# Performance work log

Measured on AMD Instinct MI355X. Metric: run time of the kernel, lower is better.

## Reference

```python
import jax, jax.numpy as jnp
import numpy as np

B, S, Lb, C, CP, H = 64, 4, 64, 32, 16, 4
LN_EPS = 1e-5


def layer_norm(x, g, b):
    mu = jnp.mean(x, axis=-1, keepdims=True)
    var = jnp.mean(jnp.square(x - mu), axis=-1, keepdims=True)
    return (x - mu) * jax.lax.rsqrt(var + LN_EPS) * g + b


def mha(x, w_in, b_in, w_out, b_out, h):
    # torch nn.MultiheadAttention, batch_first, self-attention
    Bx, L, Cx = x.shape
    d = Cx // h
    qkv = x @ w_in.T + b_in                      # (Bx, L, 3C)
    q, k, v = jnp.split(qkv, 3, axis=-1)
    sp = lambda t: t.reshape(Bx, L, h, d).transpose(0, 2, 1, 3)  # (Bx,h,L,d)
    q, k, v = sp(q), sp(k), sp(v)
    scale = 1.0 / jnp.sqrt(jnp.asarray(d, x.dtype))
    attn = jax.nn.softmax(jnp.einsum('bhid,bhjd->bhij', q, k) * scale, axis=-1)
    o = jnp.einsum('bhij,bhjd->bhid', attn, v).transpose(0, 2, 1, 3).reshape(Bx, L, Cx)
    return o @ w_out.T + b_out


def setup_inputs() -> dict:
    key = jax.random.key(0)
    ks = jax.random.split(key, 20)
    g = lambda i, shape, s=0.05: (jax.random.normal(ks[i], shape, dtype=jnp.float32) * s)
    inp = {
        'chip_ctcf': jax.random.normal(ks[0], (B, Lb), dtype=jnp.float32),
        'chip_hac':  jax.random.normal(ks[1], (B, Lb), dtype=jnp.float32),
        'chip_me1':  jax.random.normal(ks[2], (B, Lb), dtype=jnp.float32),
        'chip_me3':  jax.random.normal(ks[3], (B, Lb), dtype=jnp.float32),
        'embed_w': g(4, (C, 1)), 'embed_b': g(5, (C,)),
        'pos_embed': g(6, (1, 1, Lb, C), 0.02),
        'row_in_w': g(7, (3 * C, C)), 'row_in_b': g(8, (3 * C,)),
        'row_out_w': g(9, (C, C)), 'row_out_b': g(10, (C,)),
        'row_ln_g': jnp.ones((C,), jnp.float32), 'row_ln_b': jnp.zeros((C,), jnp.float32),
        'col_in_w': g(11, (3 * C, C)), 'col_in_b': g(12, (3 * C,)),
        'col_out_w': g(13, (C, C)), 'col_out_b': g(14, (C,)),
        'col_ln_g': jnp.ones((C,), jnp.float32), 'col_ln_b': jnp.zeros((C,), jnp.float32),
        'proj_w': g(15, (CP, C * C)), 'proj_b': g(16, (CP,)),
        'pln_g': jnp.ones((CP,), jnp.float32), 'pln_b': jnp.zeros((CP,), jnp.float32),
    }
    return inp


def reference(chip_ctcf, chip_hac, chip_me1, chip_me3,
              embed_w, embed_b, pos_embed,
              row_in_w, row_in_b, row_out_w, row_out_b, row_ln_g, row_ln_b,
              col_in_w, col_in_b, col_out_w, col_out_b, col_ln_g, col_ln_b,
              proj_w, proj_b, pln_g, pln_b):
    Bv = chip_ctcf.shape[0]
    signals = jnp.stack([chip_ctcf, chip_hac, chip_me1, chip_me3], axis=1)  # (B,4,64)
    # Linear(1, C): scalar embed
    msa = signals[..., None] * embed_w[:, 0] + embed_b                      # (B,4,64,C)
    msa = msa + pos_embed
    # row attention over the 64 bins, per track
    x = msa.reshape(Bv * S, Lb, C)
    x = layer_norm(x + mha(x, row_in_w, row_in_b, row_out_w, row_out_b, H), row_ln_g, row_ln_b)
    msa = x.reshape(Bv, S, Lb, C)
    # column attention over the 4 tracks, per bin
    x = msa.transpose(0, 2, 1, 3).reshape(Bv * Lb, S, C)
    x = layer_norm(x + mha(x, col_in_w, col_in_b, col_out_w, col_out_b, H), col_ln_g, col_ln_b)
    msa = x.reshape(Bv, Lb, S, C).transpose(0, 2, 1, 3)                     # (B,4,64,C)
    # outer product of the track-mean (as written in the torch source)
    m = jnp.mean(msa, axis=1)                                               # (B,64,C)
    pair = jnp.einsum('bic,bjd->bijcd', m, m).reshape(Bv, Lb, Lb, C * C)    # (B,64,64,1024)
    nrm = jnp.sqrt(jnp.sum(jnp.square(pair), axis=-1, keepdims=True))
    pair = pair / jnp.maximum(nrm, 1e-6)                                    # F.normalize eps=1e-6
    feat = pair @ proj_w.T + proj_b                                         # (B,64,64,CP)
    feat = layer_norm(feat, pln_g, pln_b)
    feat = feat * jax.nn.sigmoid(feat)                                      # SiLU
    return feat.transpose(0, 3, 1, 2)                                       # (B,CP,64,64)
```

## Files before the change

kernel.cpp:

```cpp
#include <hip/hip_runtime.h>
#include <hip/hip_cooperative_groups.h>

namespace cg = cooperative_groups;

#define LN_EPS 1e-5f

__device__ __forceinline__ float dot8(float4 a0, float4 a1, float4 b0, float4 b1) {
    return a0.x * b0.x + a0.y * b0.y + a0.z * b0.z + a0.w * b0.w +
           a1.x * b1.x + a1.y * b1.y + a1.z * b1.z + a1.w * b1.w;
}

__global__ __launch_bounds__(512, 4) void k_fused(
    const float* __restrict__ ctcf, const float* __restrict__ hac,
    const float* __restrict__ me1,  const float* __restrict__ me3,
    const float* __restrict__ ew,   const float* __restrict__ eb,
    const float* __restrict__ pe,
    const float* __restrict__ riw,  const float* __restrict__ rib,
    const float* __restrict__ row_w,const float* __restrict__ row_b,
    const float* __restrict__ rlg,  const float* __restrict__ rlb,
    const float* __restrict__ ciw,  const float* __restrict__ cib,
    const float* __restrict__ cow,  const float* __restrict__ cob,
    const float* __restrict__ clg,  const float* __restrict__ clb,
    const float* __restrict__ pw,   const float* __restrict__ pb,
    const float* __restrict__ pg,   const float* __restrict__ pbt,
    float* msaR, float* mbuf, float* nbuf, float* out)
{
    __shared__ float smem[7552];
    const int bx  = blockIdx.x;
    const int tid = threadIdx.x;
    cg::grid_group grid = cg::this_grid();

    {
        float* sqkv = smem;
        float* so   = smem + 6400;

        const int qh = bx & 1, s = (bx >> 1) & 3, b = bx >> 3;
        const int qbase = qh * 32;
        const float* chip = (s == 0) ? ctcf : (s == 1) ? hac : (s == 2) ? me1 : me3;
        const int l   = tid & 63;
        const int cgi = __builtin_amdgcn_readfirstlane(tid >> 6);

        float xr[32];
        {
            const float cv = chip[b * 64 + l];
            const float4* pe4 = (const float4*)&pe[l * 32];
            const float4* ew4 = (const float4*)ew;
            const float4* eb4 = (const float4*)eb;
#pragma unroll
            for (int c4 = 0; c4 < 8; ++c4) {
                float4 pv = pe4[c4], e = ew4[c4], bb = eb4[c4];
                xr[c4 * 4 + 0] = cv * e.x + bb.x + pv.x;
                xr[c4 * 4 + 1] = cv * e.y + bb.y + pv.y;
                xr[c4 * 4 + 2] = cv * e.z + bb.z + pv.z;
                xr[c4 * 4 + 3] = cv * e.w + bb.w + pv.w;
            }
        }

        {
            const int cc0 = cgi * 12;
            float acc[12];
#pragma unroll
            for (int ii = 0; ii < 12; ++ii) acc[ii] = rib[cc0 + ii];
#pragma unroll
            for (int ii = 0; ii < 12; ++ii) {
                const float4* wr4 = (const float4*)&riw[(cc0 + ii) * 32];
#pragma unroll
                for (int c4 = 0; c4 < 8; ++c4) {
                    float4 wv = wr4[c4];
                    acc[ii] += xr[c4 * 4 + 0] * wv.x + xr[c4 * 4 + 1] * wv.y +
                               xr[c4 * 4 + 2] * wv.z + xr[c4 * 4 + 3] * wv.w;
                }
            }
            float* dst = &sqkv[l * 100 + cc0];
            *(float4*)(dst + 0) = make_float4(acc[0], acc[1], acc[2],  acc[3]);
            *(float4*)(dst + 4) = make_float4(acc[4], acc[5], acc[6],  acc[7]);
            *(float4*)(dst + 8) = make_float4(acc[8], acc[9], acc[10], acc[11]);
        }
        __syncthreads();

        {
            const int h  = tid >> 7;
            const int q  = (tid >> 2) & 31;
            const int kc = tid & 3;
            const int lq = qbase + q;
            const float4* qp = (const float4*)&sqkv[lq * 100 + h * 8];
            float4 q0 = qp[0], q1 = qp[1];
            const float scale = 0.35355339059327373f;

            float sc[16];
#pragma unroll
            for (int jj = 0; jj < 16; ++jj) {
                const int j = kc * 16 + ((jj + kc) & 15);
                const float4* kp = (const float4*)&sqkv[j * 100 + 32 + h * 8];
                sc[jj] = dot8(q0, q1, kp[0], kp[1]) * scale;
            }
            float m0 = fmaxf(fmaxf(fmaxf(sc[0], sc[1]),  fmaxf(sc[2], sc[3])),
                             fmaxf(fmaxf(sc[4], sc[5]),  fmaxf(sc[6], sc[7])));
            float m1 = fmaxf(fmaxf(fmaxf(sc[8], sc[9]),  fmaxf(sc[10], sc[11])),
                             fmaxf(fmaxf(sc[12], sc[13]), fmaxf(sc[14], sc[15])));
            float mx = fmaxf(m0, m1);
            mx = fmaxf(mx, __shfl_xor(mx, 1, 64));
            mx = fmaxf(mx, __shfl_xor(mx, 2, 64));

            float den = 0.f, a[8];
#pragma unroll
            for (int dd = 0; dd < 8; ++dd) a[dd] = 0.f;
#pragma unroll
            for (int jj = 0; jj < 16; ++jj) {
                const int j = kc * 16 + ((jj + kc) & 15);
                float wgt = __expf(sc[jj] - mx);
                den += wgt;
                const float4* vp = (const float4*)&sqkv[j * 100 + 64 + h * 8];
                float4 v0 = vp[0], v1 = vp[1];
                a[0] += wgt * v0.x;  a[1] += wgt * v0.y;
                a[2] += wgt * v0.z;  a[3] += wgt * v0.w;
                a[4] += wgt * v1.x;  a[5] += wgt * v1.y;
                a[6] += wgt * v1.z;  a[7] += wgt * v1.w;
            }
#pragma unroll
            for (int off = 1; off <= 2; off <<= 1) {
                den += __shfl_xor(den, off, 64);
#pragma unroll
                for (int dd = 0; dd < 8; ++dd) a[dd] += __shfl_xor(a[dd], off, 64);
            }
            float inv = 1.f / den;
            float r0, r1;
            if      (kc == 0) { r0 = a[0]; r1 = a[1]; }
            else if (kc == 1) { r0 = a[2]; r1 = a[3]; }
            else if (kc == 2) { r0 = a[4]; r1 = a[5]; }
            else              { r0 = a[6]; r1 = a[7]; }
            so[q * 36 + h * 8 + kc * 2 + 0] = r0 * inv;
            so[q * 36 + h * 8 + kc * 2 + 1] = r1 * inv;
        }
        __syncthreads();

        {
            const int lq2 = tid & 31;
            const int cB  = tid >> 5;
            const int lg  = qbase + lq2;
            const float cvr = chip[b * 64 + lg];
            float orow[32];
            const float4* sop = (const float4*)&so[lq2 * 36];
#pragma unroll
            for (int k4 = 0; k4 < 8; ++k4) {
                float4 t = sop[k4];
                orow[k4 * 4 + 0] = t.x;  orow[k4 * 4 + 1] = t.y;
                orow[k4 * 4 + 2] = t.z;  orow[k4 * 4 + 3] = t.w;
            }
#pragma unroll
            for (int i = 0; i < 2; ++i) {
                int c = cB + i * 16;
                const float4* wr4 = (const float4*)&row_w[c * 32];
                float acc = row_b[c] + (cvr * ew[c] + eb[c] + pe[lg * 32 + c]);
#pragma unroll
                for (int k4 = 0; k4 < 8; ++k4) {
                    float4 wv = wr4[k4];
                    acc += orow[k4 * 4 + 0] * wv.x + orow[k4 * 4 + 1] * wv.y +
                           orow[k4 * 4 + 2] * wv.z + orow[k4 * 4 + 3] * wv.w;
                }
                sqkv[lq2 * 100 + c] = acc;
            }
        }
        __syncthreads();

        {
            const int c = tid & 31;
#pragma unroll
            for (int p = 0; p < 2; ++p) {
                int r = p * 16 + (tid >> 5);
                float v = sqkv[r * 100 + c];
                float s1 = v;
#pragma unroll
                for (int off = 16; off >= 1; off >>= 1) s1 += __shfl_xor(s1, off, 64);
                float mu = s1 * (1.f / 32.f);
                float d = v - mu;
                float s2 = d * d;
#pragma unroll
                for (int off = 16; off >= 1; off >>= 1) s2 += __shfl_xor(s2, off, 64);
                float rstd = rsqrtf(s2 * (1.f / 32.f) + LN_EPS);
                msaR[((b * 4 + s) * 64 + qbase + r) * 32 + c] =
                    d * rstd * rlg[c] + rlb[c];
            }
        }
    }
    grid.sync();

    {
        float* sx2   = smem;
        float* sqkv2 = smem + 1056;
        float* so2   = smem + 4256;

        const int b  = bx >> 3;
        const int l0 = (bx & 7) * 8;

        for (int n = tid; n < 1024; n += 512) {
            int r = n >> 5, c = n & 31;
            int lo = r >> 2, s = r & 3;
            sx2[r * 33 + c] = msaR[((b * 4 + s) * 64 + l0 + lo) * 32 + c];
        }
        __syncthreads();

        {
            const int rr = tid & 31;
            const int cg2 = tid >> 5;
            float xr[32];
#pragma unroll
            for (int c = 0; c < 32; ++c) xr[c] = sx2[rr * 33 + c];
#pragma unroll
            for (int i = 0; i < 6; ++i) {
                int cc = i * 16 + cg2;
                const float4* wr4 = (const float4*)&ciw[cc * 32];
                float acc = cib[cc];
#pragma unroll
                for (int c4 = 0; c4 < 8; ++c4) {
                    float4 wv = wr4[c4];
                    acc += xr[c4 * 4 + 0] * wv.x + xr[c4 * 4 + 1] * wv.y +
                           xr[c4 * 4 + 2] * wv.z + xr[c4 * 4 + 3] * wv.w;
                }
                sqkv2[rr * 100 + cc] = acc;
            }
        }
        __syncthreads();

        if (tid < 128) {
            const int lo = tid >> 4, h = (tid >> 2) & 3, ia = tid & 3;
            const float scale = 0.35355339059327373f;
            const float4* qp = (const float4*)&sqkv2[(lo * 4 + ia) * 100 + h * 8];
            float4 q0 = qp[0], q1 = qp[1];
            float sc[4];
            float mx = -1e30f;
#pragma unroll
            for (int jj = 0; jj < 4; ++jj) {
                const float4* kp = (const float4*)&sqkv2[(lo * 4 + jj) * 100 + 32 + h * 8];
                sc[jj] = dot8(q0, q1, kp[0], kp[1]) * scale;
                mx = fmaxf(mx, sc[jj]);
            }
            float den = 0.f;
#pragma unroll
            for (int jj = 0; jj < 4; ++jj) { sc[jj] = __expf(sc[jj] - mx); den += sc[jj]; }
            float inv = 1.f / den;
            float a[8];
#pragma unroll
            for (int dd = 0; dd < 8; ++dd) a[dd] = 0.f;
#pragma unroll
            for (int jj = 0; jj < 4; ++jj) {
                const float4* vp = (const float4*)&sqkv2[(lo * 4 + jj) * 100 + 64 + h * 8];
                float4 v0 = vp[0], v1 = vp[1];
                float wgt = sc[jj];
                a[0] += wgt * v0.x;  a[1] += wgt * v0.y;
                a[2] += wgt * v0.z;  a[3] += wgt * v0.w;
                a[4] += wgt * v1.x;  a[5] += wgt * v1.y;
                a[6] += wgt * v1.z;  a[7] += wgt * v1.w;
            }
#pragma unroll
            for (int dd = 0; dd < 8; ++dd) so2[(lo * 4 + ia) * 36 + h * 8 + dd] = a[dd] * inv;
        }
        __syncthreads();

        {
            const int r2 = tid & 31;
            const int cB = tid >> 5;
            float orow[32];
            const float4* sop = (const float4*)&so2[r2 * 36];
#pragma unroll
            for (int k4 = 0; k4 < 8; ++k4) {
                float4 t = sop[k4];
                orow[k4 * 4 + 0] = t.x;  orow[k4 * 4 + 1] = t.y;
                orow[k4 * 4 + 2] = t.z;  orow[k4 * 4 + 3] = t.w;
            }
#pragma unroll
            for (int i = 0; i < 2; ++i) {
                int c = cB + i * 16;
                const float4* wr4 = (const float4*)&cow[c * 32];
                float acc = cob[c] + sx2[r2 * 33 + c];
#pragma unroll
                for (int k4 = 0; k4 < 8; ++k4) {
                    float4 wv = wr4[k4];
                    acc += orow[k4 * 4 + 0] * wv.x + orow[k4 * 4 + 1] * wv.y +
                           orow[k4 * 4 + 2] * wv.z + orow[k4 * 4 + 3] * wv.w;
                }
                sqkv2[r2 * 100 + c] = acc;
            }
        }
        __syncthreads();

        {
            const int c = tid & 31;
#pragma unroll
            for (int p = 0; p < 2; ++p) {
                int r = p * 16 + (tid >> 5);
                float v = sqkv2[r * 100 + c];
                float s1 = v;
#pragma unroll
                for (int off = 16; off >= 1; off >>= 1) s1 += __shfl_xor(s1, off, 64);
                float mu = s1 * (1.f / 32.f);
                float d = v - mu;
                float s2 = d * d;
#pragma unroll
                for (int off = 16; off >= 1; off >>= 1) s2 += __shfl_xor(s2, off, 64);
                float rstd = rsqrtf(s2 * (1.f / 32.f) + LN_EPS);
                so2[r * 36 + c] = d * rstd;
            }
        }
        __syncthreads();

        if (tid < 256) {
            const int lo = tid >> 5, c = tid & 31;
            float mval = 0.25f * (so2[(lo * 4 + 0) * 36 + c] + so2[(lo * 4 + 1) * 36 + c] +
                                  so2[(lo * 4 + 2) * 36 + c] + so2[(lo * 4 + 3) * 36 + c]) *
                         clg[c] + clb[c];
            mbuf[(b * 64 + l0 + lo) * 32 + c] = mval;
            float q2 = mval * mval;
#pragma unroll
            for (int off = 16; off >= 1; off >>= 1) q2 += __shfl_xor(q2, off, 64);
            if (c == 0) nbuf[b * 64 + l0 + lo] = sqrtf(q2);
        }
    }
    grid.sync();

    {
        float* smj = smem;
        float* sT  = smem + 2304;
        float* snj = smem + 6464;
        float* sb  = smem + 6528;
        float* sg  = smem + 6544;
        float* sbt = smem + 6560;

        const int b  = bx >> 3;
        const int i0 = (bx & 7) * 8;
        const int lane = tid & 63, w = tid >> 6;

        const float* pwp = pw + (tid >> 5) * 1024 + (tid & 31);
        float w0[32];
#pragma unroll
        for (int c = 0; c < 32; ++c) w0[c] = pwp[c * 32];

        const float* mb = mbuf + b * 2048;
        for (int n = tid; n < 2048; n += 512) smj[(n >> 5) * 36 + (n & 31)] = mb[n];
        if (tid < 64) snj[tid] = nbuf[b * 64 + tid];
        if (tid < 16) { sb[tid] = pb[tid]; sg[tid] = pg[tid]; sbt[tid] = pbt[tid]; }
        __syncthreads();

#pragma unroll
        for (int il = 0; il < 8; ++il) {
            const float4* mr4 = (const float4*)&smj[(i0 + il) * 36];
            float a0 = 0.f;
#pragma unroll
            for (int c4 = 0; c4 < 8; ++c4) {
                float4 mv = mr4[c4];
                a0 += mv.x * w0[c4 * 4 + 0] + mv.y * w0[c4 * 4 + 1] +
                      mv.z * w0[c4 * 4 + 2] + mv.w * w0[c4 * 4 + 3];
            }
            sT[il * 520 + tid] = a0;
        }
        __syncthreads();

        const int j = lane;
        float mj[32];
        {
            const float4* mjp = (const float4*)&smj[j * 36];
#pragma unroll
            for (int d4 = 0; d4 < 8; ++d4) {
                float4 t = mjp[d4];
                mj[d4 * 4 + 0] = t.x;  mj[d4 * 4 + 1] = t.y;
                mj[d4 * 4 + 2] = t.z;  mj[d4 * 4 + 3] = t.w;
            }
        }
        const float nj = snj[j];
        const int il = w;
        const int ig = i0 + il;
        const float invn = 1.f / fmaxf(snj[ig] * nj, 1e-6f);
        float f[16];
#pragma unroll
        for (int cp = 0; cp < 16; ++cp) {
            const float4* tr = (const float4*)&sT[il * 520 + cp * 32];
            float acc = 0.f;
#pragma unroll
            for (int d4 = 0; d4 < 8; ++d4) {
                float4 tv = tr[d4];
                acc += tv.x * mj[d4 * 4 + 0] + tv.y * mj[d4 * 4 + 1] +
                       tv.z * mj[d4 * 4 + 2] + tv.w * mj[d4 * 4 + 3];
            }
            f[cp] = acc * invn + sb[cp];
        }
        float mu = 0.f;
#pragma unroll
        for (int cp = 0; cp < 16; ++cp) mu += f[cp];
        mu *= (1.f / 16.f);
        float var = 0.f;
#pragma unroll
        for (int cp = 0; cp < 16; ++cp) { float d = f[cp] - mu; var += d * d; }
        var *= (1.f / 16.f);
        const float rstd = rsqrtf(var + LN_EPS);
#pragma unroll
        for (int cp = 0; cp < 16; ++cp) {
            float v = (f[cp] - mu) * rstd * sg[cp] + sbt[cp];
            float sl = v / (1.f + __expf(-v));
            out[((b * 16 + cp) * 64 + ig) * 64 + j] = sl;
        }
    }
}

__global__ __launch_bounds__(512, 4) void k_row(
    const float* __restrict__ ctcf, const float* __restrict__ hac,
    const float* __restrict__ me1,  const float* __restrict__ me3,
    const float* __restrict__ ew,   const float* __restrict__ eb,
    const float* __restrict__ pe,
    const float* __restrict__ w_in, const float* __restrict__ b_in,
    const float* __restrict__ w_out,const float* __restrict__ b_out,
    const float* __restrict__ ln_g, const float* __restrict__ ln_b,
    float* __restrict__ msaR)
{
    __shared__ float sx[64][33];
    __shared__ float sqkv[64 * 100];
    __shared__ float so[32][33];

    const int blk = blockIdx.x;
    const int qh  = blk & 1;
    const int s   = (blk >> 1) & 3;
    const int b   = blk >> 3;
    const int qbase = qh * 32;
    const int tid = threadIdx.x;

    const float* chip = (s == 0) ? ctcf : (s == 1) ? hac : (s == 2) ? me1 : me3;

    const int l  = tid & 63;
    const int cg = __builtin_amdgcn_readfirstlane(tid >> 6);

    float xr[32];
    {
        const float cv = chip[b * 64 + l];
        const float4* pe4 = (const float4*)&pe[l * 32];
        const float4* ew4 = (const float4*)ew;
        const float4* eb4 = (const float4*)eb;
#pragma unroll
        for (int c4 = 0; c4 < 8; ++c4) {
            float4 pv = pe4[c4], e = ew4[c4], bb = eb4[c4];
            xr[c4 * 4 + 0] = cv * e.x + bb.x + pv.x;
            xr[c4 * 4 + 1] = cv * e.y + bb.y + pv.y;
            xr[c4 * 4 + 2] = cv * e.z + bb.z + pv.z;
            xr[c4 * 4 + 3] = cv * e.w + bb.w + pv.w;
        }
    }
    if (cg == 0) {
#pragma unroll
        for (int c = 0; c < 32; ++c) sx[l][c] = xr[c];
    }

#pragma unroll
    for (int i = 0; i < 12; ++i) {
        const int cc = i * 8 + cg;
        const float4* wr4 = (const float4*)&w_in[cc * 32];
        float acc = b_in[cc];
#pragma unroll
        for (int c4 = 0; c4 < 8; ++c4) {
            float4 wv = wr4[c4];
            acc += xr[c4 * 4 + 0] * wv.x + xr[c4 * 4 + 1] * wv.y +
                   xr[c4 * 4 + 2] * wv.z + xr[c4 * 4 + 3] * wv.w;
        }
        sqkv[l * 100 + cc] = acc;
    }
    __syncthreads();

    {
        const int h  = tid >> 7;
        const int q  = (tid >> 2) & 31;
        const int kc = tid & 3;
        const int lq = qbase + q;
        const float4* qp = (const float4*)&sqkv[lq * 100 + h * 8];
        float4 q0 = qp[0], q1 = qp[1];
        const float scale = 0.35355339059327373f;

        float sc[16];
#pragma unroll
        for (int jj = 0; jj < 16; ++jj) {
            const int j = kc * 16 + ((jj + kc) & 15);
            const float4* kp = (const float4*)&sqkv[j * 100 + 32 + h * 8];
            sc[jj] = dot8(q0, q1, kp[0], kp[1]) * scale;
        }
        float m0 = fmaxf(fmaxf(fmaxf(sc[0], sc[1]),  fmaxf(sc[2], sc[3])),
                         fmaxf(fmaxf(sc[4], sc[5]),  fmaxf(sc[6], sc[7])));
        float m1 = fmaxf(fmaxf(fmaxf(sc[8], sc[9]),  fmaxf(sc[10], sc[11])),
                         fmaxf(fmaxf(sc[12], sc[13]), fmaxf(sc[14], sc[15])));
        float mx = fmaxf(m0, m1);
        mx = fmaxf(mx, __shfl_xor(mx, 1, 64));
        mx = fmaxf(mx, __shfl_xor(mx, 2, 64));

        float den = 0.f, a[8];
#pragma unroll
        for (int dd = 0; dd < 8; ++dd) a[dd] = 0.f;
#pragma unroll
        for (int jj = 0; jj < 16; ++jj) {
            const int j = kc * 16 + ((jj + kc) & 15);
            float w = __expf(sc[jj] - mx);
            den += w;
            const float4* vp = (const float4*)&sqkv[j * 100 + 64 + h * 8];
            float4 v0 = vp[0], v1 = vp[1];
            a[0] += w * v0.x;  a[1] += w * v0.y;
            a[2] += w * v0.z;  a[3] += w * v0.w;
            a[4] += w * v1.x;  a[5] += w * v1.y;
            a[6] += w * v1.z;  a[7] += w * v1.w;
        }
#pragma unroll
        for (int off = 1; off <= 2; off <<= 1) {
            den += __shfl_xor(den, off, 64);
#pragma unroll
            for (int dd = 0; dd < 8; ++dd) a[dd] += __shfl_xor(a[dd], off, 64);
        }
        float inv = 1.f / den;
        float r0, r1;
        if      (kc == 0) { r0 = a[0]; r1 = a[1]; }
        else if (kc == 1) { r0 = a[2]; r1 = a[3]; }
        else if (kc == 2) { r0 = a[4]; r1 = a[5]; }
        else              { r0 = a[6]; r1 = a[7]; }
        so[q][h * 8 + kc * 2 + 0] = r0 * inv;
        so[q][h * 8 + kc * 2 + 1] = r1 * inv;
    }
    __syncthreads();

    {
        const int lq2 = tid & 31;
        const int cB  = tid >> 5;
        float orow[32];
#pragma unroll
        for (int k = 0; k < 32; ++k) orow[k] = so[lq2][k];
#pragma unroll
        for (int i = 0; i < 2; ++i) {
            int c = cB + i * 16;
            const float4* wr4 = (const float4*)&w_out[c * 32];
            float acc = b_out[c] + sx[qbase + lq2][c];
#pragma unroll
            for (int k4 = 0; k4 < 8; ++k4) {
                float4 wv = wr4[k4];
                acc += orow[k4 * 4 + 0] * wv.x + orow[k4 * 4 + 1] * wv.y +
                       orow[k4 * 4 + 2] * wv.z + orow[k4 * 4 + 3] * wv.w;
            }
            sqkv[lq2 * 100 + c] = acc;
        }
    }
    __syncthreads();

    {
        const int c = tid & 31;
#pragma unroll
        for (int p = 0; p < 2; ++p) {
            int r = p * 16 + (tid >> 5);
            float v = sqkv[r * 100 + c];
            float s1 = v;
#pragma unroll
            for (int off = 16; off >= 1; off >>= 1) s1 += __shfl_xor(s1, off, 64);
            float mu = s1 * (1.f / 32.f);
            float d = v - mu;
            float s2 = d * d;
#pragma unroll
            for (int off = 16; off >= 1; off >>= 1) s2 += __shfl_xor(s2, off, 64);
            float rstd = rsqrtf(s2 * (1.f / 32.f) + LN_EPS);
            msaR[((b * 4 + s) * 64 + qbase + r) * 32 + c] = d * rstd * ln_g[c] + ln_b[c];
        }
    }
}

__global__ __launch_bounds__(256, 4) void k_col(
    const float* __restrict__ msaR,
    const float* __restrict__ w_in, const float* __restrict__ b_in,
    const float* __restrict__ w_out,const float* __restrict__ b_out,
    const float* __restrict__ ln_g, const float* __restrict__ ln_b,
    float* __restrict__ m_out, float* __restrict__ nrm_out)
{
    __shared__ float sx[16][33];
    __shared__ float sqkv[16 * 100];
    __shared__ float so[16][33];

    const int bx = blockIdx.x;
    const int b  = bx >> 4;
    const int l0 = (bx & 15) * 4;
    const int tid = threadIdx.x;

    for (int n = tid; n < 512; n += 256) {
        int r = n >> 5, c = n & 31;
        int lo = r >> 2, s = r & 3;
        sx[r][c] = msaR[((b * 4 + s) * 64 + l0 + lo) * 32 + c];
    }
    __syncthreads();

    {
        const int rr = tid & 15;
        const int cg = tid >> 4;
        float xr[32];
#pragma unroll
        for (int c = 0; c < 32; ++c) xr[c] = sx[rr][c];
#pragma unroll
        for (int i = 0; i < 6; ++i) {
            int cc = i * 16 + cg;
            const float4* wr4 = (const float4*)&w_in[cc * 32];
            float acc = b_in[cc];
#pragma unroll
            for (int c4 = 0; c4 < 8; ++c4) {
                float4 wv = wr4[c4];
                acc += xr[c4 * 4 + 0] * wv.x + xr[c4 * 4 + 1] * wv.y +
                       xr[c4 * 4 + 2] * wv.z + xr[c4 * 4 + 3] * wv.w;
            }
            sqkv[rr * 100 + cc] = acc;
        }
    }
    __syncthreads();

    if (tid < 64) {
        const int lo = tid >> 4, h = (tid >> 2) & 3, ia = tid & 3;
        const float scale = 0.35355339059327373f;
        const float4* qp = (const float4*)&sqkv[(lo * 4 + ia) * 100 + h * 8];
        float4 q0 = qp[0], q1 = qp[1];
        float sc[4];
        float mx = -1e30f;
#pragma unroll
        for (int jj = 0; jj < 4; ++jj) {
            const float4* kp = (const float4*)&sqkv[(lo * 4 + jj) * 100 + 32 + h * 8];
            sc[jj] = dot8(q0, q1, kp[0], kp[1]) * scale;
            mx = fmaxf(mx, sc[jj]);
        }
        float den = 0.f;
#pragma unroll
        for (int jj = 0; jj < 4; ++jj) { sc[jj] = __expf(sc[jj] - mx); den += sc[jj]; }
        float inv = 1.f / den;
        float a[8];
#pragma unroll
        for (int dd = 0; dd < 8; ++dd) a[dd] = 0.f;
#pragma unroll
        for (int jj = 0; jj < 4; ++jj) {
            const float4* vp = (const float4*)&sqkv[(lo * 4 + jj) * 100 + 64 + h * 8];
            float4 v0 = vp[0], v1 = vp[1];
            float wgt = sc[jj];
            a[0] += wgt * v0.x;  a[1] += wgt * v0.y;
            a[2] += wgt * v0.z;  a[3] += wgt * v0.w;
            a[4] += wgt * v1.x;  a[5] += wgt * v1.y;
            a[6] += wgt * v1.z;  a[7] += wgt * v1.w;
        }
#pragma unroll
        for (int dd = 0; dd < 8; ++dd) so[lo * 4 + ia][h * 8 + dd] = a[dd] * inv;
    }
    __syncthreads();

    {
        const int r2 = tid & 15;
        const int cB = tid >> 4;
        float orow[32];
#pragma unroll
        for (int k = 0; k < 32; ++k) orow[k] = so[r2][k];
#pragma unroll
        for (int i = 0; i < 2; ++i) {
            int c = cB + i * 16;
            const float4* wr4 = (const float4*)&w_out[c * 32];
            float acc = b_out[c] + sx[r2][c];
#pragma unroll
            for (int k4 = 0; k4 < 8; ++k4) {
                float4 wv = wr4[k4];
                acc += orow[k4 * 4 + 0] * wv.x + orow[k4 * 4 + 1] * wv.y +
                       orow[k4 * 4 + 2] * wv.z + orow[k4 * 4 + 3] * wv.w;
            }
            sqkv[r2 * 100 + c] = acc;
        }
    }
    __syncthreads();

    {
        const int c = tid & 31;
#pragma unroll
        for (int p = 0; p < 2; ++p) {
            int r = p * 8 + (tid >> 5);
            float v = sqkv[r * 100 + c];
            float s1 = v;
#pragma unroll
            for (int off = 16; off >= 1; off >>= 1) s1 += __shfl_xor(s1, off, 64);
            float mu = s1 * (1.f / 32.f);
            float d = v - mu;
            float s2 = d * d;
#pragma unroll
            for (int off = 16; off >= 1; off >>= 1) s2 += __shfl_xor(s2, off, 64);
            float rstd = rsqrtf(s2 * (1.f / 32.f) + LN_EPS);
            so[r][c] = d * rstd;
        }
    }
    __syncthreads();

    if (tid < 128) {
        const int lo = tid >> 5, c = tid & 31;
        float mval = 0.25f * (so[lo * 4 + 0][c] + so[lo * 4 + 1][c] +
                              so[lo * 4 + 2][c] + so[lo * 4 + 3][c]) * ln_g[c] + ln_b[c];
        m_out[(b * 64 + l0 + lo) * 32 + c] = mval;
        float q2 = mval * mval;
#pragma unroll
        for (int off = 16; off >= 1; off >>= 1) q2 += __shfl_xor(q2, off, 64);
        if (c == 0) nrm_out[b * 64 + l0 + lo] = sqrtf(q2);
    }
}

__global__ __launch_bounds__(256, 4) void k_pair(
    const float* __restrict__ m, const float* __restrict__ nrm,
    const float* __restrict__ pw, const float* __restrict__ pb,
    const float* __restrict__ pg, const float* __restrict__ pbeta,
    float* __restrict__ out)
{
    __shared__ float smj[64][36];
    __shared__ float sT[4 * 520];
    __shared__ float snj[64];
    __shared__ float sbias[16], sgam[16], sbet[16];

    const int bx = blockIdx.x;
    const int b  = bx >> 4;
    const int i0 = (bx & 15) * 4;
    const int tid = threadIdx.x;
    const int lane = tid & 63, w = tid >> 6;

    const int rem0 = tid, rem1 = tid + 256;
    const float* pw0 = pw + (rem0 >> 5) * 1024 + (rem0 & 31);
    const float* pw1 = pw + (rem1 >> 5) * 1024 + (rem1 & 31);
    float w0[32], w1[32];
#pragma unroll
    for (int c = 0; c < 32; ++c) { w0[c] = pw0[c * 32]; w1[c] = pw1[c * 32]; }

    const float* mb = m + b * 2048;
    for (int n = tid; n < 2048; n += 256) smj[n >> 5][n & 31] = mb[n];
    if (tid < 64) snj[tid] = nrm[b * 64 + tid];
    if (tid < 16) {
        sbias[tid] = pb[tid];
        sgam[tid]  = pg[tid];
        sbet[tid]  = pbeta[tid];
    }
    __syncthreads();

#pragma unroll
    for (int il = 0; il < 4; ++il) {
        const float4* mr4 = (const float4*)&smj[i0 + il][0];
        float a0 = 0.f, a1 = 0.f;
#pragma unroll
        for (int c4 = 0; c4 < 8; ++c4) {
            float4 mv = mr4[c4];
            a0 += mv.x * w0[c4 * 4 + 0] + mv.y * w0[c4 * 4 + 1] +
                  mv.z * w0[c4 * 4 + 2] + mv.w * w0[c4 * 4 + 3];
            a1 += mv.x * w1[c4 * 4 + 0] + mv.y * w1[c4 * 4 + 1] +
                  mv.z * w1[c4 * 4 + 2] + mv.w * w1[c4 * 4 + 3];
        }
        sT[il * 520 + rem0] = a0;
        sT[il * 520 + rem1] = a1;
    }
    __syncthreads();

    const int j = lane;
    float mj[32];
    {
        const float4* mjp = (const float4*)&smj[j][0];
#pragma unroll
        for (int d4 = 0; d4 < 8; ++d4) {
            float4 t = mjp[d4];
            mj[d4 * 4 + 0] = t.x;  mj[d4 * 4 + 1] = t.y;
            mj[d4 * 4 + 2] = t.z;  mj[d4 * 4 + 3] = t.w;
        }
    }
    const float nj = snj[j];

    {
        const int il = w;
        const int ig = i0 + il;
        const float invn = 1.f / fmaxf(snj[ig] * nj, 1e-6f);
        float f[16];
#pragma unroll
        for (int cp = 0; cp < 16; ++cp) {
            const float4* tr = (const float4*)&sT[il * 520 + cp * 32];
            float acc = 0.f;
#pragma unroll
            for (int d4 = 0; d4 < 8; ++d4) {
                float4 tv = tr[d4];
                acc += tv.x * mj[d4 * 4 + 0] + tv.y * mj[d4 * 4 + 1] +
                       tv.z * mj[d4 * 4 + 2] + tv.w * mj[d4 * 4 + 3];
            }
            f[cp] = acc * invn + sbias[cp];
        }
        float mu = 0.f;
#pragma unroll
        for (int cp = 0; cp < 16; ++cp) mu += f[cp];
        mu *= (1.f / 16.f);
        float var = 0.f;
#pragma unroll
        for (int cp = 0; cp < 16; ++cp) { float d = f[cp] - mu; var += d * d; }
        var *= (1.f / 16.f);
        const float rstd = rsqrtf(var + LN_EPS);
#pragma unroll
        for (int cp = 0; cp < 16; ++cp) {
            float v = (f[cp] - mu) * rstd * sgam[cp] + sbet[cp];
            float sl = v / (1.f + __expf(-v));
            out[((b * 16 + cp) * 64 + ig) * 64 + j] = sl;
        }
    }
}

extern "C" void kernel_launch(void* const* d_in, const int* in_sizes, int n_in,
                              void* d_out, int out_size, void* d_ws, size_t ws_size,
                              hipStream_t stream) {
    const float* ctcf  = (const float*)d_in[0];
    const float* hac   = (const float*)d_in[1];
    const float* me1   = (const float*)d_in[2];
    const float* me3   = (const float*)d_in[3];
    const float* ew    = (const float*)d_in[4];
    const float* ebias = (const float*)d_in[5];
    const float* pe    = (const float*)d_in[6];
    const float* riw   = (const float*)d_in[7];
    const float* rib   = (const float*)d_in[8];
    const float* row_  = (const float*)d_in[9];
    const float* rob   = (const float*)d_in[10];
    const float* rlg   = (const float*)d_in[11];
    const float* rlb   = (const float*)d_in[12];
    const float* ciw   = (const float*)d_in[13];
    const float* cib   = (const float*)d_in[14];
    const float* cow   = (const float*)d_in[15];
    const float* cob   = (const float*)d_in[16];
    const float* clg   = (const float*)d_in[17];
    const float* clb   = (const float*)d_in[18];
    const float* pw    = (const float*)d_in[19];
    const float* pb    = (const float*)d_in[20];
    const float* pg    = (const float*)d_in[21];
    const float* pbt   = (const float*)d_in[22];

    float* outp = (float*)d_out;

    float* msaR = (float*)d_out;
    float* mbuf = (float*)d_ws;
    float* nbuf = mbuf + 64 * 64 * 32;

    static int s_coop = -1;
    if (s_coop < 0) {
        int nb = 0;
        hipError_t e = hipOccupancyMaxActiveBlocksPerMultiprocessor(
            &nb, k_fused, 512, 0);
        s_coop = (e == hipSuccess && nb >= 2) ? 1 : 0;
    }

    if (s_coop) {
        void* args[] = {
            (void*)&ctcf, (void*)&hac, (void*)&me1, (void*)&me3,
            (void*)&ew,   (void*)&ebias, (void*)&pe,
            (void*)&riw,  (void*)&rib, (void*)&row_, (void*)&rob,
            (void*)&rlg,  (void*)&rlb,
            (void*)&ciw,  (void*)&cib, (void*)&cow, (void*)&cob,
            (void*)&clg,  (void*)&clb,
            (void*)&pw,   (void*)&pb,  (void*)&pg,  (void*)&pbt,
            (void*)&msaR, (void*)&mbuf, (void*)&nbuf, (void*)&outp
        };
        hipError_t le = hipLaunchCooperativeKernel((void*)k_fused, dim3(512),
                                                   dim3(512), args, 0, stream);
        if (le != hipSuccess) s_coop = 0;
    }
    if (!s_coop) {
        k_row<<<512, 512, 0, stream>>>(ctcf, hac, me1, me3, ew, ebias, pe,
                                       riw, rib, row_, rob, rlg, rlb, msaR);
        k_col<<<1024, 256, 0, stream>>>(msaR, ciw, cib, cow, cob, clg, clb,
                                        mbuf, nbuf);
        k_pair<<<1024, 256, 0, stream>>>(mbuf, nbuf, pw, pb, pg, pbt, outp);
    }
}
```

Before: 144.8 us.

## Split pair stage out of cooperative kernel and tweak fallback row kernel

Removes the second grid.sync and pair stage from the cooperative kernel, which now covers only the row and column stages. The pair stage always runs as a separate k_pair launch with 1024 blocks of 256 threads. This swaps a grid-wide barrier for a kernel boundary and lets the pair stage use its own launch geometry. The fallback k_row also computes 12 contiguous qkv outputs per thread with vectorized stores and recomputes the residual input instead of staging it in shared memory, though that path only runs when the cooperative launch fails.

Result: no change. 142.7 us (-1.4%).

```diff
diff --git a/kernel.cpp b/kernel.cpp
--- a/kernel.cpp
+++ b/kernel.cpp
@@ -10,7 +10,7 @@
            a1.x * b1.x + a1.y * b1.y + a1.z * b1.z + a1.w * b1.w;
 }
 
-__global__ __launch_bounds__(512, 4) void k_fused(
+__global__ __launch_bounds__(512, 4) void k12(
     const float* __restrict__ ctcf, const float* __restrict__ hac,
     const float* __restrict__ me1,  const float* __restrict__ me3,
     const float* __restrict__ ew,   const float* __restrict__ eb,
@@ -21,9 +21,7 @@
     const float* __restrict__ ciw,  const float* __restrict__ cib,
     const float* __restrict__ cow,  const float* __restrict__ cob,
     const float* __restrict__ clg,  const float* __restrict__ clb,
-    const float* __restrict__ pw,   const float* __restrict__ pb,
-    const float* __restrict__ pg,   const float* __restrict__ pbt,
-    float* msaR, float* mbuf, float* nbuf, float* out)
+    float* msaR, float* mbuf, float* nbuf)
 {
     __shared__ float smem[7552];
     const int bx  = blockIdx.x;
@@ -316,89 +314,6 @@
             if (c == 0) nbuf[b * 64 + l0 + lo] = sqrtf(q2);
         }
     }
-    grid.sync();
-
-    {
-        float* smj = smem;
-        float* sT  = smem + 2304;
-        float* snj = smem + 6464;
-        float* sb  = smem + 6528;
-        float* sg  = smem + 6544;
-        float* sbt = smem + 6560;
-
-        const int b  = bx >> 3;
-        const int i0 = (bx & 7) * 8;
-        const int lane = tid & 63, w = tid >> 6;
-
-        const float* pwp = pw + (tid >> 5) * 1024 + (tid & 31);
-        float w0[32];
-#pragma unroll
-        for (int c = 0; c < 32; ++c) w0[c] = pwp[c * 32];
-
-        const float* mb = mbuf + b * 2048;
-        for (int n = tid; n < 2048; n += 512) smj[(n >> 5) * 36 + (n & 31)] = mb[n];
-        if (tid < 64) snj[tid] = nbuf[b * 64 + tid];
-        if (tid < 16) { sb[tid] = pb[tid]; sg[tid] = pg[tid]; sbt[tid] = pbt[tid]; }
-        __syncthreads();
-
-#pragma unroll
-        for (int il = 0; il < 8; ++il) {
-            const float4* mr4 = (const float4*)&smj[(i0 + il) * 36];
-            float a0 = 0.f;
-#pragma unroll
-            for (int c4 = 0; c4 < 8; ++c4) {
-                float4 mv = mr4[c4];
-                a0 += mv.x * w0[c4 * 4 + 0] + mv.y * w0[c4 * 4 + 1] +
-                      mv.z * w0[c4 * 4 + 2] + mv.w * w0[c4 * 4 + 3];
-            }
-            sT[il * 520 + tid] = a0;
-        }
-        __syncthreads();
-
-        const int j = lane;
-        float mj[32];
-        {
-            const float4* mjp = (const float4*)&smj[j * 36];
-#pragma unroll
-            for (int d4 = 0; d4 < 8; ++d4) {
-                float4 t = mjp[d4];
-                mj[d4 * 4 + 0] = t.x;  mj[d4 * 4 + 1] = t.y;
-                mj[d4 * 4 + 2] = t.z;  mj[d4 * 4 + 3] = t.w;
-            }
-        }
-        const float nj = snj[j];
-        const int il = w;
-        const int ig = i0 + il;
-        const float invn = 1.f / fmaxf(snj[ig] * nj, 1e-6f);
-        float f[16];
-#pragma unroll
-        for (int cp = 0; cp < 16; ++cp) {
-            const float4* tr = (const float4*)&sT[il * 520 + cp * 32];
-            float acc = 0.f;
-#pragma unroll
-            for (int d4 = 0; d4 < 8; ++d4) {
-                float4 tv = tr[d4];
-                acc += tv.x * mj[d4 * 4 + 0] + tv.y * mj[d4 * 4 + 1] +
-                       tv.z * mj[d4 * 4 + 2] + tv.w * mj[d4 * 4 + 3];
-            }
-            f[cp] = acc * invn + sb[cp];
-        }
-        float mu = 0.f;
-#pragma unroll
-        for (int cp = 0; cp < 16; ++cp) mu += f[cp];
-        mu *= (1.f / 16.f);
-        float var = 0.f;
-#pragma unroll
-        for (int cp = 0; cp < 16; ++cp) { float d = f[cp] - mu; var += d * d; }
-        var *= (1.f / 16.f);
-        const float rstd = rsqrtf(var + LN_EPS);
-#pragma unroll
-        for (int cp = 0; cp < 16; ++cp) {
-            float v = (f[cp] - mu) * rstd * sg[cp] + sbt[cp];
-            float sl = v / (1.f + __expf(-v));
-            out[((b * 16 + cp) * 64 + ig) * 64 + j] = sl;
-        }
-    }
 }
 
 __global__ __launch_bounds__(512, 4) void k_row(
@@ -411,9 +326,8 @@
     const float* __restrict__ ln_g, const float* __restrict__ ln_b,
     float* __restrict__ msaR)
 {
-    __shared__ float sx[64][33];
     __shared__ float sqkv[64 * 100];
-    __shared__ float so[32][33];
+    __shared__ float so[32][36];
 
     const int blk = blockIdx.x;
     const int qh  = blk & 1;
@@ -442,23 +356,26 @@
             xr[c4 * 4 + 3] = cv * e.w + bb.w + pv.w;
         }
     }
-    if (cg == 0) {
-#pragma unroll
-        for (int c = 0; c < 32; ++c) sx[l][c] = xr[c];
-    }
-
-#pragma unroll
-    for (int i = 0; i < 12; ++i) {
-        const int cc = i * 8 + cg;
-        const float4* wr4 = (const float4*)&w_in[cc * 32];
-        float acc = b_in[cc];
-#pragma unroll
-        for (int c4 = 0; c4 < 8; ++c4) {
-            float4 wv = wr4[c4];
-            acc += xr[c4 * 4 + 0] * wv.x + xr[c4 * 4 + 1] * wv.y +
-                   xr[c4 * 4 + 2] * wv.z + xr[c4 * 4 + 3] * wv.w;
-        }
-        sqkv[l * 100 + cc] = acc;
+
+    {
+        const int cc0 = cg * 12;
+        float acc[12];
+#pragma unroll
+        for (int ii = 0; ii < 12; ++ii) acc[ii] = b_in[cc0 + ii];
+#pragma unroll
+        for (int ii = 0; ii < 12; ++ii) {
+            const float4* wr4 = (const float4*)&w_in[(cc0 + ii) * 32];
+#pragma unroll
+            for (int c4 = 0; c4 < 8; ++c4) {
+                float4 wv = wr4[c4];
+                acc[ii] += xr[c4 * 4 + 0] * wv.x + xr[c4 * 4 + 1] * wv.y +
+                           xr[c4 * 4 + 2] * wv.z + xr[c4 * 4 + 3] * wv.w;
+            }
+        }
+        float* dst = &sqkv[l * 100 + cc0];
+        *(float4*)(dst + 0) = make_float4(acc[0], acc[1], acc[2],  acc[3]);
+        *(float4*)(dst + 4) = make_float4(acc[4], acc[5], acc[6],  acc[7]);
+        *(float4*)(dst + 8) = make_float4(acc[8], acc[9], acc[10], acc[11]);
     }
     __syncthreads();
 
@@ -521,14 +438,21 @@
     {
         const int lq2 = tid & 31;
         const int cB  = tid >> 5;
+        const int lg  = qbase + lq2;
+        const float cvr = chip[b * 64 + lg];
         float orow[32];
-#pragma unroll
-        for (int k = 0; k < 32; ++k) orow[k] = so[lq2][k];
+        const float4* sop = (const float4*)&so[lq2][0];
+#pragma unroll
+        for (int k4 = 0; k4 < 8; ++k4) {
+            float4 t = sop[k4];
+            orow[k4 * 4 + 0] = t.x;  orow[k4 * 4 + 1] = t.y;
+            orow[k4 * 4 + 2] = t.z;  orow[k4 * 4 + 3] = t.w;
+        }
 #pragma unroll
         for (int i = 0; i < 2; ++i) {
             int c = cB + i * 16;
             const float4* wr4 = (const float4*)&w_out[c * 32];
-            float acc = b_out[c] + sx[qbase + lq2][c];
+            float acc = b_out[c] + (cvr * ew[c] + eb[c] + pe[lg * 32 + c]);
 #pragma unroll
             for (int k4 = 0; k4 < 8; ++k4) {
                 float4 wv = wr4[k4];
@@ -830,10 +754,11 @@
     if (s_coop < 0) {
         int nb = 0;
         hipError_t e = hipOccupancyMaxActiveBlocksPerMultiprocessor(
-            &nb, k_fused, 512, 0);
+            &nb, k12, 512, 0);
         s_coop = (e == hipSuccess && nb >= 2) ? 1 : 0;
     }
 
+    bool done12 = false;
     if (s_coop) {
         void* args[] = {
             (void*)&ctcf, (void*)&hac, (void*)&me1, (void*)&me3,
@@ -842,18 +767,17 @@
             (void*)&rlg,  (void*)&rlb,
             (void*)&ciw,  (void*)&cib, (void*)&cow, (void*)&cob,
             (void*)&clg,  (void*)&clb,
-            (void*)&pw,   (void*)&pb,  (void*)&pg,  (void*)&pbt,
-            (void*)&msaR, (void*)&mbuf, (void*)&nbuf, (void*)&outp
+            (void*)&msaR, (void*)&mbuf, (void*)&nbuf
         };
-        hipError_t le = hipLaunchCooperativeKernel((void*)k_fused, dim3(512),
+        hipError_t le = hipLaunchCooperativeKernel((void*)k12, dim3(512),
                                                    dim3(512), args, 0, stream);
-        if (le != hipSuccess) s_coop = 0;
-    }
-    if (!s_coop) {
+        if (le == hipSuccess) done12 = true; else s_coop = 0;
+    }
+    if (!done12) {
         k_row<<<512, 512, 0, stream>>>(ctcf, hac, me1, me3, ew, ebias, pe,
                                        riw, rib, row_, rob, rlg, rlb, msaR);
         k_col<<<1024, 256, 0, stream>>>(msaR, ciw, cib, cow, cob, clg, clb,
                                         mbuf, nbuf);
-        k_pair<<<1024, 256, 0, stream>>>(mbuf, nbuf, pw, pb, pg, pbt, outp);
-    }
+    }
+    k_pair<<<1024, 256, 0, stream>>>(mbuf, nbuf, pw, pb, pg, pbt, outp);
 }
```
